# Kernel tuning notes

Hardware: AMD Instinct MI355X
Metric: run time of the kernel (lower is better)

The kernel has to match this reference:

```python
import jax, jax.numpy as jnp
import numpy as np

D_MODEL = 1024
NUM_HEADS = 16
D_K = D_MODEL // NUM_HEADS
LOCAL_WINDOW = 3
STRIDE = 4


def strided_mask(seq_len):
    # position i attends to j iff j <= i and (i-j <= local_window or (i-j) % stride == 0)
    i = jnp.arange(seq_len)[:, None]
    j = jnp.arange(seq_len)[None, :]
    d = i - j
    return (d >= 0) & ((d <= LOCAL_WINDOW) | (d % STRIDE == 0))


def setup_inputs() -> dict:
    key = jax.random.key(0)
    ks = jax.random.split(key, 11)
    B, S, D = 4, 1024, D_MODEL
    s = 1.0 / np.sqrt(D)
    inp = {
        "Q": jax.random.normal(ks[0], (B, S, D), jnp.float32),
        "K": jax.random.normal(ks[1], (B, S, D), jnp.float32),
        "V": jax.random.normal(ks[2], (B, S, D), jnp.float32),
        "Wq": jax.random.normal(ks[3], (D, D), jnp.float32) * s,
        "bq": jnp.zeros((D,), jnp.float32),
        "Wk": jax.random.normal(ks[4], (D, D), jnp.float32) * s,
        "bk": jnp.zeros((D,), jnp.float32),
        "Wv": jax.random.normal(ks[5], (D, D), jnp.float32) * s,
        "bv": jnp.zeros((D,), jnp.float32),
        "Wo": jax.random.normal(ks[6], (D, D), jnp.float32) * s,
        "bo": jnp.zeros((D,), jnp.float32),
    }
    return inp


def reference(Q, K, V, Wq, bq, Wk, bk, Wv, bv, Wo, bo):
    B, S, D = Q.shape
    H, dk = NUM_HEADS, D_K

    def split(x):  # [B,S,D] -> [B,H,S,dk]
        return x.reshape(B, S, H, dk).transpose(0, 2, 1, 3)

    q = split(Q @ Wq + bq)
    k = split(K @ Wk + bk)
    v = split(V @ Wv + bv)

    scores = jnp.einsum("bhsd,bhtd->bhst", q, k) / jnp.sqrt(
        jnp.asarray(dk, jnp.float32))
    m = strided_mask(S)[None, None]  # [1,1,S,S]
    scores = jnp.where(m, scores, -1e9)
    attn = jax.nn.softmax(scores, axis=-1)
    out = jnp.einsum("bhst,bhtd->bhsd", attn, v)
    out = out.transpose(0, 2, 1, 3).reshape(B, S, D)  # combine heads
    return out @ Wo + bo
```

## Files before the change

kernel.cpp:

```cpp
#include <hip/hip_runtime.h>

typedef _Float16 f16;
typedef __attribute__((ext_vector_type(8))) _Float16 f16x8;
typedef __attribute__((ext_vector_type(4))) _Float16 f16x4;
typedef __attribute__((ext_vector_type(4))) float f32x4;

#define MFMA16(a, b, c) __builtin_amdgcn_mfma_f32_16x16x32_f16((a), (b), (c), 0, 0, 0)

__device__ __forceinline__ void gld_lds16(const void* g, void* l) {
  __builtin_amdgcn_global_load_lds(
      (__attribute__((address_space(1))) void*)const_cast<void*>(g),
      (__attribute__((address_space(3))) void*)l, 16, 0, 0);
}

__device__ __forceinline__ f16x8 ld8(const f16* p) { return *(const f16x8*)p; }

__global__ __launch_bounds__(256) void cvt_x_kernel(
    const float* __restrict__ Q, const float* __restrict__ K, const float* __restrict__ V,
    f16* __restrict__ oq, f16* __restrict__ ok, f16* __restrict__ ov) {
  const float* src = blockIdx.z == 0 ? Q : (blockIdx.z == 1 ? K : V);
  f16* dst = blockIdx.z == 0 ? oq : (blockIdx.z == 1 ? ok : ov);
  size_t i = ((size_t)blockIdx.x * 256 + threadIdx.x) * 4;
  float4 f = *(const float4*)(src + i);
  f16x4 o4;
  o4.x = (f16)f.x; o4.y = (f16)f.y; o4.z = (f16)f.z; o4.w = (f16)f.w;
  *(f16x4*)(dst + i) = o4;
}

__global__ __launch_bounds__(256) void cvt_wT_kernel(
    const float* __restrict__ Wq, const float* __restrict__ Wk,
    const float* __restrict__ Wv, const float* __restrict__ Wo,
    f16* __restrict__ Tq, f16* __restrict__ Tk, f16* __restrict__ Tv, f16* __restrict__ To) {
  const int z = blockIdx.z;
  const float* W = z == 0 ? Wq : (z == 1 ? Wk : (z == 2 ? Wv : Wo));
  f16* T = z == 0 ? Tq : (z == 1 ? Tk : (z == 2 ? Tv : To));
  __shared__ float tile[64][65];
  const int k0 = blockIdx.x * 64, n0 = blockIdx.y * 64;
  const int tx = threadIdx.x & 63, ty = threadIdx.x >> 6;
#pragma unroll
  for (int rr = 0; rr < 16; ++rr) {
    int r = rr * 4 + ty;
    tile[r][tx] = W[(size_t)(k0 + r) * 1024 + n0 + tx];
  }
  __syncthreads();
#pragma unroll
  for (int rr = 0; rr < 16; ++rr) {
    int nn = rr * 4 + ty;
    T[(size_t)(n0 + nn) * 1024 + k0 + tx] = (f16)tile[tx][nn];
  }
}

template <bool QKV>
__global__ __launch_bounds__(256) void gemm_bt_kernel(
    const f16* __restrict__ A0, const f16* __restrict__ A1, const f16* __restrict__ A2,
    const f16* __restrict__ B0, const f16* __restrict__ B1, const f16* __restrict__ B2,
    const float* __restrict__ bias0, const float* __restrict__ bias1, const float* __restrict__ bias2,
    f16* __restrict__ C0, f16* __restrict__ C1, f16* __restrict__ C2,
    f16* __restrict__ C3, float* __restrict__ Cf) {
  const int z = blockIdx.z;
  const f16* A = z == 0 ? A0 : (z == 1 ? A1 : A2);
  const f16* Bt = z == 0 ? B0 : (z == 1 ? B1 : B2);
  const float* bias = z == 0 ? bias0 : (z == 1 ? bias1 : bias2);

  __shared__ alignas(16) f16 lA[128 * 32];
  __shared__ alignas(16) f16 lB[128 * 32];

  const int t = threadIdx.x;
  const int w = t >> 6, lane = t & 63, quad = lane >> 4, l15 = lane & 15;
  const int wm = w >> 1, wn = w & 1;
  const int mbase = blockIdx.x * 128;
  const int nbase = blockIdx.y * 128;

  const f32x4 zero4 = {0.f, 0.f, 0.f, 0.f};
  f32x4 acc[4][4];
#pragma unroll
  for (int mi = 0; mi < 4; ++mi)
#pragma unroll
    for (int ni = 0; ni < 4; ++ni) acc[mi][ni] = zero4;

  const int r = t >> 2;
  const int koff = (t & 3) * 8;

  for (int k0 = 0; k0 < 1024; k0 += 32) {
    __syncthreads();
    gld_lds16(A + (size_t)(mbase + r) * 1024 + k0 + koff, (char*)lA + w * 1024);
    gld_lds16(A + (size_t)(mbase + 64 + r) * 1024 + k0 + koff, (char*)lA + 4096 + w * 1024);
    gld_lds16(Bt + (size_t)(nbase + r) * 1024 + k0 + koff, (char*)lB + w * 1024);
    gld_lds16(Bt + (size_t)(nbase + 64 + r) * 1024 + k0 + koff, (char*)lB + 4096 + w * 1024);
    __syncthreads();

    f16x8 af[4], bf[4];
#pragma unroll
    for (int mi = 0; mi < 4; ++mi)
      af[mi] = ld8(&lA[(wm * 64 + mi * 16 + l15) * 32 + quad * 8]);
#pragma unroll
    for (int ni = 0; ni < 4; ++ni)
      bf[ni] = ld8(&lB[(wn * 64 + ni * 16 + l15) * 32 + quad * 8]);
#pragma unroll
    for (int mi = 0; mi < 4; ++mi)
#pragma unroll
      for (int ni = 0; ni < 4; ++ni)
        acc[mi][ni] = MFMA16(af[mi], bf[ni], acc[mi][ni]);
  }

#pragma unroll
  for (int mi = 0; mi < 4; ++mi) {
#pragma unroll
    for (int ni = 0; ni < 4; ++ni) {
#pragma unroll
      for (int rg = 0; rg < 4; ++rg) {
        const int row = mbase + wm * 64 + mi * 16 + quad * 4 + rg;
        const int col = nbase + wn * 64 + ni * 16 + l15;
        const float v = acc[mi][ni][rg] + bias[col];
        if (QKV) {
          const int bh = (row >> 10) * 16 + (col >> 6);
          const int s = row & 1023, d = col & 63;
          const f16 hv = (f16)v;
          if (z != 2) {
            f16* Ch = (z == 0) ? C0 : C1;
            Ch[(size_t)bh * 65536 + s * 64 + d] = hv;
          } else {
            C2[(size_t)bh * 65536 + s * 64 + d] = hv;
            const int rr = s & 3, n = s >> 2, wi = n & 63;
            C3[(size_t)bh * 65536 + (size_t)rr * 16384 + (size_t)d * 256 +
               (n & ~63) + ((wi & 15) << 2) + (wi >> 4)] = hv;
          }
        } else {
          Cf[(size_t)row * 1024 + col] = v;
        }
      }
    }
  }
}

__global__ __launch_bounds__(256) void attn_far_kernel(
    const f16* __restrict__ qh, const f16* __restrict__ kh,
    const f16* __restrict__ vtg, float* __restrict__ po, float* __restrict__ ml) {
  const int t = threadIdx.x;
  const int w = t >> 6, lane = t & 63, quad = lane >> 4, l15 = lane & 15;
  const int widx = blockIdx.x + 512 * w;
  const int bh = (widx & 255) >> 2, r = widx & 3;
  const int wq = widx >> 8;
  const int m0 = wq * 32;
  const int ntiles = (wq >> 1) + 1;

  __shared__ alignas(16) f16 lp[4][2][16 * 72];

  const f16* qb = qh + (size_t)bh * 65536;
  const f16* kb = kh + (size_t)bh * 65536;
  const f16* vb = vtg + (size_t)bh * 65536 + (size_t)r * 16384;
  const float SCL2 = 0.125f * 1.44269504f;

  f16x8 aq[2][2];
#pragma unroll
  for (int mt = 0; mt < 2; ++mt) {
    const int i = 4 * (m0 + mt * 16 + l15) + r;
#pragma unroll
    for (int ko = 0; ko < 2; ++ko)
      aq[mt][ko] = ld8(qb + (size_t)i * 64 + ko * 32 + quad * 8);
  }

  const f32x4 zero4 = {0.f, 0.f, 0.f, 0.f};
  f32x4 o[2][4];
  float mrun[2][4], lrun[2][4];
#pragma unroll
  for (int mt = 0; mt < 2; ++mt)
#pragma unroll
    for (int i = 0; i < 4; ++i) {
      o[mt][i] = zero4; mrun[mt][i] = -1e30f; lrun[mt][i] = 0.f;
    }

  for (int jt = 0; jt < ntiles; ++jt) {
    const int n0 = jt * 64;
    f16x8 bk0[4], bk1[4], bv0[4], bv1[4];
#pragma unroll
    for (int nt = 0; nt < 4; ++nt) {
      const f16* kr = kb + (size_t)(4 * (n0 + nt * 16 + l15) + r) * 64;
      bk0[nt] = ld8(kr + quad * 8);
      bk1[nt] = ld8(kr + 32 + quad * 8);
      const f16* vr = vb + (size_t)(nt * 16 + l15) * 256 + n0;
      bv0[nt] = ld8(vr + quad * 8);
      bv1[nt] = ld8(vr + 32 + quad * 8);
    }
    const bool lastt = (jt == ntiles - 1);
#pragma unroll
    for (int mt = 0; mt < 2; ++mt) {
      f32x4 sc[4];
#pragma unroll
      for (int nt = 0; nt < 4; ++nt) {
        f32x4 c = MFMA16(aq[mt][0], bk0[nt], zero4);
        sc[nt] = MFMA16(aq[mt][1], bk1[nt], c);
      }
#pragma unroll
      for (int rg = 0; rg < 4; ++rg) {
        const int m = m0 + mt * 16 + quad * 4 + rg;
        float s[4];
#pragma unroll
        for (int nt = 0; nt < 4; ++nt) {
          float vsc = sc[nt][rg] * SCL2;
          if (lastt) vsc = (n0 + nt * 16 + l15 < m) ? vsc : -3.0e38f;
          s[nt] = vsc;
        }
        float tm = fmaxf(fmaxf(s[0], s[1]), fmaxf(s[2], s[3]));
        tm = fmaxf(tm, __shfl_xor(tm, 1));
        tm = fmaxf(tm, __shfl_xor(tm, 2));
        tm = fmaxf(tm, __shfl_xor(tm, 4));
        tm = fmaxf(tm, __shfl_xor(tm, 8));
        const float mnew = fmaxf(mrun[mt][rg], tm);
        const float alpha = exp2f(mrun[mt][rg] - mnew);
        float p[4], ps = 0.f;
#pragma unroll
        for (int nt = 0; nt < 4; ++nt) { p[nt] = exp2f(s[nt] - mnew); ps += p[nt]; }
        ps += __shfl_xor(ps, 1);
        ps += __shfl_xor(ps, 2);
        ps += __shfl_xor(ps, 4);
        ps += __shfl_xor(ps, 8);
        lrun[mt][rg] = lrun[mt][rg] * alpha + ps;
        mrun[mt][rg] = mnew;
#pragma unroll
        for (int ntv = 0; ntv < 4; ++ntv) o[mt][ntv][rg] *= alpha;
        f16x4 pk;
        pk.x = (f16)p[0]; pk.y = (f16)p[1]; pk.z = (f16)p[2]; pk.w = (f16)p[3];
        *(f16x4*)&lp[w][mt][(quad * 4 + rg) * 72 + l15 * 4] = pk;
      }
    }
#pragma unroll
    for (int mt = 0; mt < 2; ++mt) {
      const f16x8 ap0 = ld8(&lp[w][mt][l15 * 72 + quad * 8]);
      const f16x8 ap1 = ld8(&lp[w][mt][l15 * 72 + 32 + quad * 8]);
#pragma unroll
      for (int ntv = 0; ntv < 4; ++ntv) {
        f32x4 c = MFMA16(ap0, bv0[ntv], o[mt][ntv]);
        o[mt][ntv] = MFMA16(ap1, bv1[ntv], c);
      }
    }
  }

#pragma unroll
  for (int mt = 0; mt < 2; ++mt)
#pragma unroll
    for (int rg = 0; rg < 4; ++rg) {
      const int i = 4 * (m0 + mt * 16 + quad * 4 + rg) + r;
      const size_t idx = (size_t)bh * 1024 + i;
#pragma unroll
      for (int ntv = 0; ntv < 4; ++ntv)
        po[idx * 64 + ntv * 16 + l15] = o[mt][ntv][rg];
      if (l15 == 0) { ml[idx * 2] = mrun[mt][rg]; ml[idx * 2 + 1] = lrun[mt][rg]; }
    }
}

__global__ __launch_bounds__(256) void attn_diag_kernel(
    const f16* __restrict__ qh, const f16* __restrict__ kh, const f16* __restrict__ vh,
    const float* __restrict__ po, const float* __restrict__ ml, f16* __restrict__ ao) {
  const int t = threadIdx.x;
  const int widx = blockIdx.x * 4 + (t >> 6);
  const int l = t & 63;
  const int bh = widx >> 10, i = widx & 1023;
  const float SCL2 = 0.125f * 1.44269504f;

  const float q = (float)qh[(size_t)bh * 65536 + (size_t)i * 64 + l];
  float s[4];
#pragma unroll
  for (int d = 0; d < 4; ++d) {
    const int j = i - d;
    const int jc = j < 0 ? 0 : j;
    float pr = q * (float)kh[(size_t)bh * 65536 + (size_t)jc * 64 + l];
    pr += __shfl_xor(pr, 1);
    pr += __shfl_xor(pr, 2);
    pr += __shfl_xor(pr, 4);
    pr += __shfl_xor(pr, 8);
    pr += __shfl_xor(pr, 16);
    pr += __shfl_xor(pr, 32);
    s[d] = (j >= 0) ? pr * SCL2 : -3.0e38f;
  }
  const float md = fmaxf(fmaxf(s[0], s[1]), fmaxf(s[2], s[3]));
  const size_t idx = (size_t)bh * 1024 + i;
  const float mf = ml[idx * 2], lf = ml[idx * 2 + 1];
  const float M = fmaxf(md, mf);
  float p[4], ld = 0.f;
#pragma unroll
  for (int d = 0; d < 4; ++d) { p[d] = exp2f(s[d] - M); ld += p[d]; }
  float ov = 0.f;
#pragma unroll
  for (int d = 0; d < 4; ++d) {
    const int jc = (i - d) < 0 ? 0 : (i - d);
    ov += p[d] * (float)vh[(size_t)bh * 65536 + (size_t)jc * 64 + l];
  }
  const float fs = exp2f(mf - M);
  const float lt = lf * fs + ld;
  const float of = po[idx * 64 + l];
  const float res = (of * fs + ov) / lt;
  const int b = bh >> 4, h = bh & 15;
  ao[((size_t)(b * 1024 + i)) * 1024 + h * 64 + l] = (f16)res;
}

extern "C" void kernel_launch(void* const* d_in, const int* in_sizes, int n_in,
                              void* d_out, int out_size, void* d_ws, size_t ws_size,
                              hipStream_t stream) {
  const float* Q = (const float*)d_in[0];
  const float* K = (const float*)d_in[1];
  const float* V = (const float*)d_in[2];
  const float* Wq = (const float*)d_in[3];
  const float* bq = (const float*)d_in[4];
  const float* Wk = (const float*)d_in[5];
  const float* bk = (const float*)d_in[6];
  const float* Wv = (const float*)d_in[7];
  const float* bv = (const float*)d_in[8];
  const float* Wo = (const float*)d_in[9];
  const float* bo = (const float*)d_in[10];
  float* out = (float*)d_out;

  char* ws = (char*)d_ws;
  const size_t MB = 1ull << 20;
  f16* Xq  = (f16*)(ws + 0 * MB);
  f16* Xk  = (f16*)(ws + 8 * MB);
  f16* Xv  = (f16*)(ws + 16 * MB);
  f16* TWq = (f16*)(ws + 24 * MB);
  f16* TWk = (f16*)(ws + 26 * MB);
  f16* TWv = (f16*)(ws + 28 * MB);
  f16* TWo = (f16*)(ws + 30 * MB);
  f16* qhb = (f16*)(ws + 32 * MB);
  f16* khb = (f16*)(ws + 40 * MB);
  f16* vhb = (f16*)(ws + 48 * MB);
  f16* vtg = (f16*)(ws + 56 * MB);
  float* po  = (float*)(ws + 0 * MB);
  float* mlb = (float*)(ws + 16 * MB);
  f16* aob   = (f16*)(ws + 17 * MB);

  cvt_x_kernel<<<dim3(4096, 1, 3), 256, 0, stream>>>(Q, K, V, Xq, Xk, Xv);
  cvt_wT_kernel<<<dim3(16, 16, 4), 256, 0, stream>>>(Wq, Wk, Wv, Wo, TWq, TWk, TWv, TWo);
  gemm_bt_kernel<true><<<dim3(32, 8, 3), 256, 0, stream>>>(
      Xq, Xk, Xv, TWq, TWk, TWv, bq, bk, bv, qhb, khb, vhb, vtg, nullptr);
  attn_far_kernel<<<dim3(512), 256, 0, stream>>>(qhb, khb, vtg, po, mlb);
  attn_diag_kernel<<<dim3(16384), 256, 0, stream>>>(qhb, khb, vhb, po, mlb, aob);
  gemm_bt_kernel<false><<<dim3(32, 8, 1), 256, 0, stream>>>(
      aob, aob, aob, TWo, TWo, TWo, bo, bo, bo, nullptr, nullptr, nullptr, nullptr, out);
}
```

Baseline: 227.1 us.

## Fuse input fp16 conversion into QKV GEMM, regroup K layout, shrink out-GEMM tile

Drops the separate fp32→fp16 conversion pass over Q/K/V. The QKV GEMM now reads fp32 activations directly, converts them in registers with a one-step register prefetch, and stores them to LDS. The GEMM also writes a second K copy grouped by residue (s mod 4), so the far-attention kernel reads contiguous K rows instead of stride-4 rows. The output projection becomes a dedicated kernel with a 64-row tile, doubling the block count for better CU occupancy. In exchange, the A-operand load is synchronous rather than async global-to-LDS, and there are extra K writes plus a reshuffled workspace with aliasing between buffers.

```diff
diff --git a/kernel.cpp b/kernel.cpp
--- a/kernel.cpp
+++ b/kernel.cpp
@@ -15,16 +15,11 @@
 
 __device__ __forceinline__ f16x8 ld8(const f16* p) { return *(const f16x8*)p; }
 
-__global__ __launch_bounds__(256) void cvt_x_kernel(
-    const float* __restrict__ Q, const float* __restrict__ K, const float* __restrict__ V,
-    f16* __restrict__ oq, f16* __restrict__ ok, f16* __restrict__ ov) {
-  const float* src = blockIdx.z == 0 ? Q : (blockIdx.z == 1 ? K : V);
-  f16* dst = blockIdx.z == 0 ? oq : (blockIdx.z == 1 ? ok : ov);
-  size_t i = ((size_t)blockIdx.x * 256 + threadIdx.x) * 4;
-  float4 f = *(const float4*)(src + i);
-  f16x4 o4;
-  o4.x = (f16)f.x; o4.y = (f16)f.y; o4.z = (f16)f.z; o4.w = (f16)f.w;
-  *(f16x4*)(dst + i) = o4;
+__device__ __forceinline__ f16x8 cvt8(const float4& a, const float4& b) {
+  f16x8 h;
+  h[0] = (f16)a.x; h[1] = (f16)a.y; h[2] = (f16)a.z; h[3] = (f16)a.w;
+  h[4] = (f16)b.x; h[5] = (f16)b.y; h[6] = (f16)b.z; h[7] = (f16)b.w;
+  return h;
 }
 
 __global__ __launch_bounds__(256) void cvt_wT_kernel(
@@ -50,17 +45,16 @@
   }
 }
 
-template <bool QKV>
-__global__ __launch_bounds__(256) void gemm_bt_kernel(
-    const f16* __restrict__ A0, const f16* __restrict__ A1, const f16* __restrict__ A2,
-    const f16* __restrict__ B0, const f16* __restrict__ B1, const f16* __restrict__ B2,
-    const float* __restrict__ bias0, const float* __restrict__ bias1, const float* __restrict__ bias2,
-    f16* __restrict__ C0, f16* __restrict__ C1, f16* __restrict__ C2,
-    f16* __restrict__ C3, float* __restrict__ Cf) {
+__global__ __launch_bounds__(256) void gemm_qkv_kernel(
+    const float* __restrict__ Q32, const float* __restrict__ K32, const float* __restrict__ V32,
+    const f16* __restrict__ Bq, const f16* __restrict__ Bk, const f16* __restrict__ Bv,
+    const float* __restrict__ bq, const float* __restrict__ bk, const float* __restrict__ bv,
+    f16* __restrict__ qh, f16* __restrict__ kh, f16* __restrict__ kg,
+    f16* __restrict__ vh, f16* __restrict__ vtg) {
   const int z = blockIdx.z;
-  const f16* A = z == 0 ? A0 : (z == 1 ? A1 : A2);
-  const f16* Bt = z == 0 ? B0 : (z == 1 ? B1 : B2);
-  const float* bias = z == 0 ? bias0 : (z == 1 ? bias1 : bias2);
+  const float* A32 = z == 0 ? Q32 : (z == 1 ? K32 : V32);
+  const f16* Bt = z == 0 ? Bq : (z == 1 ? Bk : Bv);
+  const float* bias = z == 0 ? bq : (z == 1 ? bk : bv);
 
   __shared__ alignas(16) f16 lA[128 * 32];
   __shared__ alignas(16) f16 lB[128 * 32];
@@ -80,13 +74,26 @@
 
   const int r = t >> 2;
   const int koff = (t & 3) * 8;
+  const float* ap0 = A32 + (size_t)(mbase + r) * 1024 + koff;
+  const float* ap1 = A32 + (size_t)(mbase + 64 + r) * 1024 + koff;
+
+  float4 pa0 = *(const float4*)(ap0);
+  float4 pa1 = *(const float4*)(ap0 + 4);
+  float4 pb0 = *(const float4*)(ap1);
+  float4 pb1 = *(const float4*)(ap1 + 4);
 
   for (int k0 = 0; k0 < 1024; k0 += 32) {
     __syncthreads();
-    gld_lds16(A + (size_t)(mbase + r) * 1024 + k0 + koff, (char*)lA + w * 1024);
-    gld_lds16(A + (size_t)(mbase + 64 + r) * 1024 + k0 + koff, (char*)lA + 4096 + w * 1024);
+    *(f16x8*)((char*)lA + t * 16) = cvt8(pa0, pa1);
+    *(f16x8*)((char*)lA + 4096 + t * 16) = cvt8(pb0, pb1);
     gld_lds16(Bt + (size_t)(nbase + r) * 1024 + k0 + koff, (char*)lB + w * 1024);
     gld_lds16(Bt + (size_t)(nbase + 64 + r) * 1024 + k0 + koff, (char*)lB + 4096 + w * 1024);
+    if (k0 + 32 < 1024) {
+      pa0 = *(const float4*)(ap0 + k0 + 32);
+      pa1 = *(const float4*)(ap0 + k0 + 36);
+      pb0 = *(const float4*)(ap1 + k0 + 32);
+      pb1 = *(const float4*)(ap1 + k0 + 36);
+    }
     __syncthreads();
 
     f16x8 af[4], bf[4];
@@ -112,29 +119,82 @@
         const int row = mbase + wm * 64 + mi * 16 + quad * 4 + rg;
         const int col = nbase + wn * 64 + ni * 16 + l15;
         const float v = acc[mi][ni][rg] + bias[col];
-        if (QKV) {
-          const int bh = (row >> 10) * 16 + (col >> 6);
-          const int s = row & 1023, d = col & 63;
-          const f16 hv = (f16)v;
-          if (z != 2) {
-            f16* Ch = (z == 0) ? C0 : C1;
-            Ch[(size_t)bh * 65536 + s * 64 + d] = hv;
-          } else {
-            C2[(size_t)bh * 65536 + s * 64 + d] = hv;
-            const int rr = s & 3, n = s >> 2, wi = n & 63;
-            C3[(size_t)bh * 65536 + (size_t)rr * 16384 + (size_t)d * 256 +
-               (n & ~63) + ((wi & 15) << 2) + (wi >> 4)] = hv;
-          }
+        const int bh = (row >> 10) * 16 + (col >> 6);
+        const int s = row & 1023, d = col & 63;
+        const f16 hv = (f16)v;
+        if (z == 0) {
+          qh[(size_t)bh * 65536 + s * 64 + d] = hv;
+        } else if (z == 1) {
+          kh[(size_t)bh * 65536 + s * 64 + d] = hv;
+          kg[(((size_t)bh * 4 + (s & 3)) * 256 + (s >> 2)) * 64 + d] = hv;
         } else {
-          Cf[(size_t)row * 1024 + col] = v;
+          vh[(size_t)bh * 65536 + s * 64 + d] = hv;
+          const int rr = s & 3, n = s >> 2, wi = n & 63;
+          vtg[(size_t)bh * 65536 + (size_t)rr * 16384 + (size_t)d * 256 +
+              (n & ~63) + ((wi & 15) << 2) + (wi >> 4)] = hv;
         }
       }
     }
   }
 }
 
+__global__ __launch_bounds__(256) void gemm_out_kernel(
+    const f16* __restrict__ A, const f16* __restrict__ Bt,
+    const float* __restrict__ bias, float* __restrict__ Cf) {
+  __shared__ alignas(16) f16 lA[64 * 32];
+  __shared__ alignas(16) f16 lB[128 * 32];
+
+  const int t = threadIdx.x;
+  const int w = t >> 6, lane = t & 63, quad = lane >> 4, l15 = lane & 15;
+  const int wm = w >> 1, wn = w & 1;
+  const int mbase = blockIdx.x * 64;
+  const int nbase = blockIdx.y * 128;
+
+  const f32x4 zero4 = {0.f, 0.f, 0.f, 0.f};
+  f32x4 acc[2][4];
+#pragma unroll
+  for (int mi = 0; mi < 2; ++mi)
+#pragma unroll
+    for (int ni = 0; ni < 4; ++ni) acc[mi][ni] = zero4;
+
+  const int r = t >> 2;
+  const int koff = (t & 3) * 8;
+
+  for (int k0 = 0; k0 < 1024; k0 += 32) {
+    __syncthreads();
+    gld_lds16(A + (size_t)(mbase + r) * 1024 + k0 + koff, (char*)lA + w * 1024);
+    gld_lds16(Bt + (size_t)(nbase + r) * 1024 + k0 + koff, (char*)lB + w * 1024);
+    gld_lds16(Bt + (size_t)(nbase + 64 + r) * 1024 + k0 + koff, (char*)lB + 4096 + w * 1024);
+    __syncthreads();
+
+    f16x8 af[2], bf[4];
+#pragma unroll
+    for (int mi = 0; mi < 2; ++mi)
+      af[mi] = ld8(&lA[(wm * 32 + mi * 16 + l15) * 32 + quad * 8]);
+#pragma unroll
+    for (int ni = 0; ni < 4; ++ni)
+      bf[ni] = ld8(&lB[(wn * 64 + ni * 16 + l15) * 32 + quad * 8]);
+#pragma unroll
+    for (int mi = 0; mi < 2; ++mi)
+#pragma unroll
+      for (int ni = 0; ni < 4; ++ni)
+        acc[mi][ni] = MFMA16(af[mi], bf[ni], acc[mi][ni]);
+  }
+
+#pragma unroll
+  for (int mi = 0; mi < 2; ++mi)
+#pragma unroll
+    for (int ni = 0; ni < 4; ++ni)
+#pragma unroll
+      for (int rg = 0; rg < 4; ++rg) {
+        const int row = mbase + wm * 32 + mi * 16 + quad * 4 + rg;
+        const int col = nbase + wn * 64 + ni * 16 + l15;
+        Cf[(size_t)row * 1024 + col] = acc[mi][ni][rg] + bias[col];
+      }
+}
+
 __global__ __launch_bounds__(256) void attn_far_kernel(
-    const f16* __restrict__ qh, const f16* __restrict__ kh,
+    const f16* __restrict__ qh, const f16* __restrict__ kg,
     const f16* __restrict__ vtg, float* __restrict__ po, float* __restrict__ ml) {
   const int t = threadIdx.x;
   const int w = t >> 6, lane = t & 63, quad = lane >> 4, l15 = lane & 15;
@@ -147,7 +207,7 @@
   __shared__ alignas(16) f16 lp[4][2][16 * 72];
 
   const f16* qb = qh + (size_t)bh * 65536;
-  const f16* kb = kh + (size_t)bh * 65536;
+  const f16* kb = kg + ((size_t)bh * 4 + r) * 16384;
   const f16* vb = vtg + (size_t)bh * 65536 + (size_t)r * 16384;
   const float SCL2 = 0.125f * 1.44269504f;
 
@@ -175,7 +235,7 @@
     f16x8 bk0[4], bk1[4], bv0[4], bv1[4];
 #pragma unroll
     for (int nt = 0; nt < 4; ++nt) {
-      const f16* kr = kb + (size_t)(4 * (n0 + nt * 16 + l15) + r) * 64;
+      const f16* kr = kb + (size_t)(n0 + nt * 16 + l15) * 64;
       bk0[nt] = ld8(kr + quad * 8);
       bk1[nt] = ld8(kr + 32 + quad * 8);
       const f16* vr = vb + (size_t)(nt * 16 + l15) * 256 + n0;
@@ -312,27 +372,23 @@
 
   char* ws = (char*)d_ws;
   const size_t MB = 1ull << 20;
-  f16* Xq  = (f16*)(ws + 0 * MB);
-  f16* Xk  = (f16*)(ws + 8 * MB);
-  f16* Xv  = (f16*)(ws + 16 * MB);
-  f16* TWq = (f16*)(ws + 24 * MB);
-  f16* TWk = (f16*)(ws + 26 * MB);
-  f16* TWv = (f16*)(ws + 28 * MB);
-  f16* TWo = (f16*)(ws + 30 * MB);
-  f16* qhb = (f16*)(ws + 32 * MB);
-  f16* khb = (f16*)(ws + 40 * MB);
-  f16* vhb = (f16*)(ws + 48 * MB);
-  f16* vtg = (f16*)(ws + 56 * MB);
-  float* po  = (float*)(ws + 0 * MB);
-  float* mlb = (float*)(ws + 16 * MB);
-  f16* aob   = (f16*)(ws + 17 * MB);
-
-  cvt_x_kernel<<<dim3(4096, 1, 3), 256, 0, stream>>>(Q, K, V, Xq, Xk, Xv);
+  f16* TWo = (f16*)(ws + 0 * MB);
+  f16* TWq = (f16*)(ws + 2 * MB);
+  f16* TWk = (f16*)(ws + 4 * MB);
+  f16* TWv = (f16*)(ws + 6 * MB);
+  f16* qhb = (f16*)(ws + 8 * MB);
+  f16* khb = (f16*)(ws + 16 * MB);
+  f16* vhb = (f16*)(ws + 24 * MB);
+  f16* vtg = (f16*)(ws + 32 * MB);
+  f16* kgb = (f16*)(ws + 40 * MB);
+  float* po = (float*)(ws + 48 * MB);
+  float* mlb = (float*)(ws + 2 * MB);
+  f16* aob = (f16*)(ws + 32 * MB);
+
   cvt_wT_kernel<<<dim3(16, 16, 4), 256, 0, stream>>>(Wq, Wk, Wv, Wo, TWq, TWk, TWv, TWo);
-  gemm_bt_kernel<true><<<dim3(32, 8, 3), 256, 0, stream>>>(
-      Xq, Xk, Xv, TWq, TWk, TWv, bq, bk, bv, qhb, khb, vhb, vtg, nullptr);
-  attn_far_kernel<<<dim3(512), 256, 0, stream>>>(qhb, khb, vtg, po, mlb);
+  gemm_qkv_kernel<<<dim3(32, 8, 3), 256, 0, stream>>>(
+      Q, K, V, TWq, TWk, TWv, bq, bk, bv, qhb, khb, kgb, vhb, vtg);
+  attn_far_kernel<<<dim3(512), 256, 0, stream>>>(qhb, kgb, vtg, po, mlb);
   attn_diag_kernel<<<dim3(16384), 256, 0, stream>>>(qhb, khb, vhb, po, mlb, aob);
-  gemm_bt_kernel<false><<<dim3(32, 8, 1), 256, 0, stream>>>(
-      aob, aob, aob, TWo, TWo, TWo, bo, bo, bo, nullptr, nullptr, nullptr, nullptr, out);
-}
+  gemm_out_kernel<<<dim3(64, 8), 256, 0, stream>>>(aob, TWo, bo, out);
+}
```

Measured after the change: 249.3 us. +9.8%, slower.
